# Optimization experiments

Hardware: AMD Instinct MI355X
Metric: run time of the kernel (lower is better)

## Reference

```python
import jax, jax.numpy as jnp
import numpy as np

DIM = 512
NUM_ITEM = 2048
K = 10


def setup_inputs() -> dict:
    key = jax.random.key(0)
    k1, k2, k3 = jax.random.split(key, 3)
    input1 = jax.random.normal(k1, (16, DIM, 32, 32), dtype=jnp.float32)
    input2 = jax.random.normal(k2, (16, DIM, 32, 32), dtype=jnp.float32)
    stdv = 1.0 / np.sqrt(DIM)
    mempool = jax.random.uniform(k3, (NUM_ITEM, DIM), minval=-stdv, maxval=stdv, dtype=jnp.float32)
    return {"input1": input1, "input2": input2, "mempool": mempool}


def _memorize(x, mempool):
    # x: [B, C, H, W] with C == DIM
    B, C, H, W = x.shape
    q = jnp.transpose(x, (0, 2, 3, 1)).reshape(-1, C)      # [N, C]
    att = jax.nn.softmax(q @ mempool.T, axis=1)            # [N, num_item]
    val, idx = jax.lax.top_k(att, K)                       # [N, K]
    val = jax.nn.softmax(val, axis=1)                      # renormalize top-k
    # scatter(val into zeros) @ mempool == gather rows of mempool and combine
    out = jnp.einsum('nk,nkd->nd', val, mempool[idx])      # [N, C]
    return jnp.transpose(out.reshape(B, H, W, C), (0, 3, 1, 2))


def reference(input1, input2, mempool):
    return (_memorize(input1, mempool), _memorize(input2, mempool))
```

## Files before the change

### kernel.cpp

```cpp
#include <hip/hip_runtime.h>
#include <math.h>

typedef __attribute__((ext_vector_type(4))) float f4;
typedef __attribute__((ext_vector_type(8))) _Float16 f16x8;
typedef __attribute__((ext_vector_type(8))) short bf16x8;
typedef __attribute__((ext_vector_type(4))) unsigned short u16x4;
typedef unsigned int u32;
typedef unsigned short u16;

#define DIMC  512
#define NITEM 2048
#define TK    10
#define WSP   (NITEM * DIMC)
#define XWSP  (32 * DIMC * 1024)
#define QWS_OFF (3 * WSP)

#define TPB    512
#define PXB    64
#define RIT    256
#define NRND   8
#define NSLICE 16

#define MP_PL  16384
#define Q_B    49152
#define Q_PL   4096
#define SSTR   66
#define LDS_BYTES 67584
#define MV_F 0
#define MI_F 5120
#define MM_F 10240
#define MS_F 10752
#define WB_F 11264
#define IB_F 11904

#define QB_SZ  12288

#define KSWZ(i) (((i) ^ ((i) >> 2)) & 3)

union h16 { _Float16 h; u16 u; };

__device__ __forceinline__ u32 bf16_rne(float f) {
    u32 u = __float_as_uint(f);
    return (u + 0x7fffu + ((u >> 16) & 1u)) >> 16;
}

__device__ __forceinline__ void split3(float f, u16& ph, u16& pb, u16& pr) {
    h16 a; a.h = (_Float16)f;
    float f0 = (float)a.h;
    ph = a.u;
    pb = (u16)bf16_rne(f);
    pr = (u16)bf16_rne(f - f0);
}

__global__ __launch_bounds__(256)
void preconv_kernel(const float* __restrict__ mp, u16* __restrict__ ws)
{
    int idx = (blockIdx.x * 256 + threadIdx.x) * 4;
    int i  = idx >> 9;
    int k0 = idx & 511;
    f4 v = *(const f4*)(mp + (size_t)i * 512 + k0);
    int s  = k0 >> 5, kl = k0 & 31;
    int lh = (kl >> 2) & 3, pair = kl >> 4;
    u16x4 pH, pB, pR;
#pragma unroll
    for (int e = 0; e < 4; ++e) {
        u16 h, b, r; split3(v[e], h, b, r);
        pH[e] = h; pB[e] = b; pR[e] = r;
    }
    size_t base = (size_t)(i >> 4) * 8192 + (size_t)s * 512
                + (size_t)(lh * 16 + (i & 15)) * 8 + pair * 4;
    *(u16x4*)(ws + 0 * WSP + base) = pH;
    *(u16x4*)(ws + 1 * WSP + base) = pB;
    *(u16x4*)(ws + 2 * WSP + base) = pR;
}

__global__ __launch_bounds__(256)
void preconv_x_kernel(const float* __restrict__ x0, const float* __restrict__ x1,
                      u16* __restrict__ ws)
{
    int T   = blockIdx.x * 256 + threadIdx.x;
    int px  = T & 1023;
    int c4  = (T >> 10) & 127;
    int img = T >> 17;
    const float* x = (img < 16) ? x0 : x1;
    const float* src = x + ((size_t)(img & 15) * 512 + (size_t)c4 * 4) * 1024 + px;
    int s = c4 >> 3, pair = (c4 >> 2) & 1, lh = c4 & 3;
    u16x4 pH, pB, pR;
#pragma unroll
    for (int j = 0; j < 4; ++j) {
        u16 h, b, r; split3(src[(size_t)j * 1024], h, b, r);
        pH[j] = h; pB[j] = b; pR[j] = r;
    }
    size_t base = (size_t)QWS_OFF
                + (size_t)(img * 64 + (px >> 4)) * 8192 + (size_t)s * 512
                + (size_t)((lh * 16 + (px & 15)) << 3) + pair * 4;
    *(u16x4*)(ws + base + 0 * (size_t)XWSP) = pH;
    *(u16x4*)(ws + base + 1 * (size_t)XWSP) = pB;
    *(u16x4*)(ws + base + 2 * (size_t)XWSP) = pR;
}

__global__ __launch_bounds__(TPB, 4)
void memorize_v11(const float* __restrict__ mp, const u16* __restrict__ ws,
                  float* __restrict__ out)
{
    extern __shared__ char ldsb[];
    float* ldsf = (float*)ldsb;

    const int t    = threadIdx.x;
    const int lane = t & 63;
    const int w    = t >> 6;
    const int blk  = blockIdx.x;
    const int img  = blk >> 4;
    const int n0   = (blk & 15) * PXB;

    float* ob = out + (img < 16 ? (size_t)0 : (size_t)16 * DIMC * 1024)
                    + (size_t)(img & 15) * (DIMC * 1024);

    const int l15 = lane & 15;
    const int lh  = lane >> 4;
    const int ksw = lh ^ KSWZ(l15);

    const int qp = t & 63;
    const int g  = t >> 6;

    float tv[TK]; int tix[TK];
#pragma unroll
    for (int q = 0; q < TK; ++q) { tv[q] = -INFINITY; tix[q] = 0x7fffffff; }
    float rm = -INFINITY, rs = 0.0f;

    const int permL = ((((lane & 3) ^ KSWZ(lane >> 2)) << 4) + (lane >> 2)) << 3;

    const int Gx = img * 64 + (blk & 15) * 4 + w;
    const u16* bsrc0 = ws + (size_t)QWS_OFF + ((size_t)Gx << 13) + permL;

    const char* qb = ldsb + Q_B + (l15 << 6) + (ksw << 4);
    const char* ab = ldsb + (size_t)((w << 5) + l15) * 64 + (ksw << 4);

#pragma unroll 1
    for (int r = 0; r < NRND; ++r) {
        f4 acc[2][4];
#pragma unroll
        for (int mt = 0; mt < 2; ++mt)
#pragma unroll
            for (int nt = 0; nt < 4; ++nt) acc[mt][nt] = (f4){0.f, 0.f, 0.f, 0.f};

#pragma unroll 1
        for (int s = 0; s < NSLICE; ++s) {
            __syncthreads();

#pragma unroll
            for (int p = 0; p < 3; ++p) {
#pragma unroll
                for (int gg = 0; gg < 2; ++gg) {
                    const u16* src = ws + (size_t)p * WSP
                                   + ((size_t)(r * 16 + w * 2 + gg) << 13)
                                   + (s << 9) + permL;
                    char* dst = ldsb + p * MP_PL + ((w << 5) + (gg << 4)) * 64;
                    __builtin_amdgcn_global_load_lds(
                        (const __attribute__((address_space(1))) u32*)src,
                        (__attribute__((address_space(3))) u32*)dst, 16, 0, 0);
                }
            }
            if (w < 4) {
#pragma unroll
                for (int p = 0; p < 3; ++p) {
                    const u16* src = bsrc0 + (size_t)p * XWSP + (s << 9);
                    char* dst = ldsb + Q_B + p * Q_PL + (w << 10);
                    __builtin_amdgcn_global_load_lds(
                        (const __attribute__((address_space(1))) u32*)src,
                        (__attribute__((address_space(3))) u32*)dst, 16, 0, 0);
                }
            }
            __syncthreads();

            f16x8  bqH[4];
            bf16x8 bqB[4], bqR[4];
#pragma unroll
            for (int nt = 0; nt < 4; ++nt) {
                bqH[nt] = *(const f16x8*) (qb + 0 * Q_PL + nt * 1024);
                bqB[nt] = *(const bf16x8*)(qb + 1 * Q_PL + nt * 1024);
                bqR[nt] = *(const bf16x8*)(qb + 2 * Q_PL + nt * 1024);
            }
#pragma unroll
            for (int mt = 0; mt < 2; ++mt) {
                f16x8  aH = *(const f16x8*) (ab + 0 * MP_PL + mt * 1024);
                bf16x8 aB = *(const bf16x8*)(ab + 1 * MP_PL + mt * 1024);
                bf16x8 aR = *(const bf16x8*)(ab + 2 * MP_PL + mt * 1024);
#pragma unroll
                for (int nt = 0; nt < 4; ++nt) {
                    f4 c = acc[mt][nt];
                    c = __builtin_amdgcn_mfma_f32_16x16x32_f16 (aH, bqH[nt], c, 0, 0, 0);
                    c = __builtin_amdgcn_mfma_f32_16x16x32_bf16(aB, bqR[nt], c, 0, 0, 0);
                    c = __builtin_amdgcn_mfma_f32_16x16x32_bf16(aR, bqB[nt], c, 0, 0, 0);
                    acc[mt][nt] = c;
                }
            }
        }

        __syncthreads();
#pragma unroll
        for (int mt = 0; mt < 2; ++mt) {
#pragma unroll
            for (int nt = 0; nt < 4; ++nt) {
                int row = (w << 5) + (mt << 4) + (lh << 2);
                int col = (nt << 4) + l15;
                float* sp = ldsf + row * SSTR + col;
                sp[0 * SSTR] = acc[mt][nt][0];
                sp[1 * SSTR] = acc[mt][nt][1];
                sp[2 * SSTR] = acc[mt][nt][2];
                sp[3 * SSTR] = acc[mt][nt][3];
            }
        }
        __syncthreads();

        float mloc = rm;
#pragma unroll 4
        for (int jj = 0; jj < 32; ++jj) {
            int   il = (g << 5) + jj;
            float v  = ldsf[il * SSTR + qp];
            mloc = fmaxf(mloc, v);
            if (v > tv[TK - 1]) {
                int   id = r * RIT + il;
                float cv = v; int ci = id;
#pragma unroll
                for (int q = 0; q < TK; ++q) {
                    bool  gt = cv > tv[q];
                    float nv = gt ? tv[q]  : cv;
                    int   ni = gt ? tix[q] : ci;
                    tv[q]  = gt ? cv : tv[q];
                    tix[q] = gt ? ci : tix[q];
                    cv = nv; ci = ni;
                }
            }
        }
        rs *= __expf(rm - mloc);
        rm = mloc;
#pragma unroll 4
        for (int jj = 0; jj < 32; ++jj) {
            int   il = (g << 5) + jj;
            float v  = ldsf[il * SSTR + qp];
            rs += __expf(v - rm);
        }
    }

    __syncthreads();
    {
#pragma unroll
        for (int q = 0; q < TK; ++q) {
            ldsf[MV_F + (qp * 8 + g) * TK + q] = tv[q];
            ldsf[MI_F + (qp * 8 + g) * TK + q] = __int_as_float(tix[q]);
        }
        ldsf[MM_F + qp * 8 + g] = rm;
        ldsf[MS_F + qp * 8 + g] = rs;
    }
    __syncthreads();

    if (t < 64) {
        const int p = t;
        float gm[8], gs[8];
#pragma unroll
        for (int G = 0; G < 8; ++G) {
            gm[G] = ldsf[MM_F + p * 8 + G];
            gs[G] = ldsf[MS_F + p * 8 + G];
        }
        float mstar = gm[0];
#pragma unroll
        for (int G = 1; G < 8; ++G) mstar = fmaxf(mstar, gm[G]);
        float Z = 0.0f;
#pragma unroll
        for (int G = 0; G < 8; ++G) Z += gs[G] * __expf(gm[G] - mstar);

        int h0=0,h1=0,h2=0,h3=0,h4=0,h5=0,h6=0,h7=0;
        float ov[TK]; int oi[TK];
#pragma unroll
        for (int o = 0; o < TK; ++o) {
            float bv = -INFINITY; int bi = 0x7fffffff; int bg = 0;
#define SEL(G, HG)                                                               \
            {                                                                    \
                float v  = ldsf[MV_F + (p * 8 + G) * TK + (HG)];                 \
                int   id = __float_as_int(ldsf[MI_F + (p * 8 + G) * TK + (HG)]); \
                if (v > bv || (v == bv && id < bi)) { bv = v; bi = id; bg = G; } \
            }
            SEL(0, h0) SEL(1, h1) SEL(2, h2) SEL(3, h3)
            SEL(4, h4) SEL(5, h5) SEL(6, h6) SEL(7, h7)
#undef SEL
            ov[o] = bv; oi[o] = bi;
            h0 += (bg == 0); h1 += (bg == 1); h2 += (bg == 2); h3 += (bg == 3);
            h4 += (bg == 4); h5 += (bg == 5); h6 += (bg == 6); h7 += (bg == 7);
        }
        float pv[TK];
#pragma unroll
        for (int o = 0; o < TK; ++o) pv[o] = __expf(ov[o] - mstar) / Z;
        float pmax = pv[0];
        float wgt[TK]; float W = 0.0f;
#pragma unroll
        for (int o = 0; o < TK; ++o) { wgt[o] = __expf(pv[o] - pmax); W += wgt[o]; }
#pragma unroll
        for (int o = 0; o < TK; ++o) {
            ldsf[WB_F + p * TK + o] = wgt[o] / W;
            ldsf[IB_F + p * TK + o] = __int_as_float(oi[o]);
        }
    }
    __syncthreads();

    {
        const int ep = t & 63, cg = t >> 6;
        float wr[TK]; const float* rows[TK];
#pragma unroll
        for (int o = 0; o < TK; ++o) {
            wr[o]   = ldsf[WB_F + ep * TK + o];
            rows[o] = mp + (size_t)__float_as_int(ldsf[IB_F + ep * TK + o]) * DIMC;
        }
        float* obase = ob + n0 + ep;
#pragma unroll 4
        for (int cc = 0; cc < 16; ++cc) {
            int c = cg * 64 + cc * 4;
            f4 a = {0.0f, 0.0f, 0.0f, 0.0f};
#pragma unroll
            for (int o = 0; o < TK; ++o) {
                f4 rv = *(const f4*)(rows[o] + c);
#pragma unroll
                for (int z = 0; z < 4; ++z) a[z] = fmaf(wr[o], rv[z], a[z]);
            }
#pragma unroll
            for (int z = 0; z < 4; ++z) obase[(size_t)(c + z) * 1024] = a[z];
        }
    }
}

__global__ __launch_bounds__(TPB, 4)
void memorize_fb(const float* __restrict__ x0, const float* __restrict__ x1,
                 const float* __restrict__ mp, const u16* __restrict__ ws,
                 float* __restrict__ out)
{
    extern __shared__ char ldsb[];
    float* ldsf = (float*)ldsb;

    const int t    = threadIdx.x;
    const int lane = t & 63;
    const int w    = t >> 6;
    const int blk  = blockIdx.x;
    const int img  = blk >> 4;
    const int n0   = (blk & 15) * PXB;
    const int b    = img & 15;

    const float* x  = (img < 16) ? x0 : x1;
    const float* xb = x + (size_t)b * (DIMC * 1024);
    float* ob = out + (img < 16 ? (size_t)0 : (size_t)16 * DIMC * 1024)
                    + (size_t)b * (DIMC * 1024);

    const int l15 = lane & 15;
    const int lh  = lane >> 4;
    const int ksw = lh ^ KSWZ(l15);
    const int ig  = w >> 1;
    const int pg  = w & 1;
    const int qp = t & 63;
    const int g  = t >> 6;

    float tv[TK]; int tix[TK];
#pragma unroll
    for (int q = 0; q < TK; ++q) { tv[q] = -INFINITY; tix[q] = 0x7fffffff; }
    float rm = -INFINITY, rs = 0.0f;

    const int scl  = t & 31;
    const int spx  = (t >> 5) << 2;
    const int spos = (((scl >> 2) & 3) << 3) + ((scl >> 4) << 2) + (scl & 3);
    const int sslot = spos >> 3;
    const int soff  = (spos & 7) << 1;

    const u16* aw = ws + (size_t)lane * 8 + (size_t)(ig * 4) * 8192;
    const int qfb = (pg << 11) + (l15 << 6) + (ksw << 4);

#define STAGE_Q(S, BUF)                                                        \
    {                                                                          \
        const float* src = xb + (size_t)(((S) << 5) + scl) * 1024 + n0 + spx;  \
        f4 v = *(const f4*)src;                                                \
        _Pragma("unroll")                                                      \
        for (int e = 0; e < 4; ++e) {                                          \
            int px = spx + e;                                                  \
            u16 h, bb, rr; split3(v[e], h, bb, rr);                            \
            int ro = (BUF) * QB_SZ + (px << 6)                                 \
                   + (((sslot ^ KSWZ(px)) << 4) | soff);                       \
            *(u16*)(ldsb + ro)            = h;                                 \
            *(u16*)(ldsb + ro + Q_PL)     = bb;                                \
            *(u16*)(ldsb + ro + 2 * Q_PL) = rr;                                \
        }                                                                      \
    }

#define ALOADF(IT, S)                                                          \
    {                                                                          \
        const u16* ap = ar + ((size_t)(IT) << 13) + ((S) << 9);                \
        aH[IT] = *(const f16x8*) (ap + 0 * WSP);                               \
        aB[IT] = *(const bf16x8*)(ap + 1 * WSP);                               \
        aR[IT] = *(const bf16x8*)(ap + 2 * WSP);                               \
    }

#pragma unroll 1
    for (int r = 0; r < NRND; ++r) {
        const u16* ar = aw + ((size_t)r << 17);
        f4 acc[4][2];
#pragma unroll
        for (int it = 0; it < 4; ++it)
#pragma unroll
            for (int pt = 0; pt < 2; ++pt) acc[it][pt] = (f4){0.f, 0.f, 0.f, 0.f};

        __syncthreads();
        STAGE_Q(0, 0)
        __syncthreads();

#pragma unroll 1
        for (int s = 0; s < NSLICE; ++s) {
            const int cur = s & 1;
            f16x8 aH[4]; bf16x8 aB[4], aR[4];
            ALOADF(0, s)
            ALOADF(1, s)
            if (s + 1 < NSLICE) STAGE_Q(s + 1, cur ^ 1)

            const char* qc = ldsb + cur * QB_SZ + qfb;
            f16x8 qH[2]; bf16x8 qB[2], qR[2];
#pragma unroll
            for (int pt = 0; pt < 2; ++pt) {
                qH[pt] = *(const f16x8*) (qc + 0 * Q_PL + pt * 1024);
                qB[pt] = *(const bf16x8*)(qc + 1 * Q_PL + pt * 1024);
                qR[pt] = *(const bf16x8*)(qc + 2 * Q_PL + pt * 1024);
            }
#pragma unroll
            for (int it = 0; it < 4; ++it) {
                if (it < 2) ALOADF(it + 2, s)
#pragma unroll
                for (int pt = 0; pt < 2; ++pt) {
                    f4 c = acc[it][pt];
                    c = __builtin_amdgcn_mfma_f32_16x16x32_f16 (aH[it], qH[pt], c, 0, 0, 0);
                    c = __builtin_amdgcn_mfma_f32_16x16x32_bf16(aB[it], qR[pt], c, 0, 0, 0);
                    c = __builtin_amdgcn_mfma_f32_16x16x32_bf16(aR[it], qB[pt], c, 0, 0, 0);
                    acc[it][pt] = c;
                }
            }
            __syncthreads();
        }

#pragma unroll
        for (int it = 0; it < 4; ++it) {
#pragma unroll
            for (int pt = 0; pt < 2; ++pt) {
                int row = (ig << 6) + (it << 4) + (lh << 2);
                int col = (pg << 5) + (pt << 4) + l15;
                float* sp = ldsf + row * SSTR + col;
                sp[0 * SSTR] = acc[it][pt][0];
                sp[1 * SSTR] = acc[it][pt][1];
                sp[2 * SSTR] = acc[it][pt][2];
                sp[3 * SSTR] = acc[it][pt][3];
            }
        }
        __syncthreads();

        float mloc = rm;
#pragma unroll 4
        for (int jj = 0; jj < 32; ++jj) {
            int   il = (g << 5) + jj;
            float v  = ldsf[il * SSTR + qp];
            mloc = fmaxf(mloc, v);
            if (v > tv[TK - 1]) {
                int   id = r * RIT + il;
                float cv = v; int ci = id;
#pragma unroll
                for (int q = 0; q < TK; ++q) {
                    bool  gt = cv > tv[q];
                    float nv = gt ? tv[q]  : cv;
                    int   ni = gt ? tix[q] : ci;
                    tv[q]  = gt ? cv : tv[q];
                    tix[q] = gt ? ci : tix[q];
                    cv = nv; ci = ni;
                }
            }
        }
        rs *= __expf(rm - mloc);
        rm = mloc;
#pragma unroll 4
        for (int jj = 0; jj < 32; ++jj) {
            int   il = (g << 5) + jj;
            float v  = ldsf[il * SSTR + qp];
            rs += __expf(v - rm);
        }
    }
#undef STAGE_Q
#undef ALOADF

    __syncthreads();
    {
#pragma unroll
        for (int q = 0; q < TK; ++q) {
            ldsf[MV_F + (qp * 8 + g) * TK + q] = tv[q];
            ldsf[MI_F + (qp * 8 + g) * TK + q] = __int_as_float(tix[q]);
        }
        ldsf[MM_F + qp * 8 + g] = rm;
        ldsf[MS_F + qp * 8 + g] = rs;
    }
    __syncthreads();

    if (t < 64) {
        const int p = t;
        float gm[8], gs[8];
#pragma unroll
        for (int G = 0; G < 8; ++G) {
            gm[G] = ldsf[MM_F + p * 8 + G];
            gs[G] = ldsf[MS_F + p * 8 + G];
        }
        float mstar = gm[0];
#pragma unroll
        for (int G = 1; G < 8; ++G) mstar = fmaxf(mstar, gm[G]);
        float Z = 0.0f;
#pragma unroll
        for (int G = 0; G < 8; ++G) Z += gs[G] * __expf(gm[G] - mstar);

        int h0=0,h1=0,h2=0,h3=0,h4=0,h5=0,h6=0,h7=0;
        float ov[TK]; int oi[TK];
#pragma unroll
        for (int o = 0; o < TK; ++o) {
            float bv = -INFINITY; int bi = 0x7fffffff; int bg = 0;
#define SEL(G, HG)                                                               \
            {                                                                    \
                float v  = ldsf[MV_F + (p * 8 + G) * TK + (HG)];                 \
                int   id = __float_as_int(ldsf[MI_F + (p * 8 + G) * TK + (HG)]); \
                if (v > bv || (v == bv && id < bi)) { bv = v; bi = id; bg = G; } \
            }
            SEL(0, h0) SEL(1, h1) SEL(2, h2) SEL(3, h3)
            SEL(4, h4) SEL(5, h5) SEL(6, h6) SEL(7, h7)
#undef SEL
            ov[o] = bv; oi[o] = bi;
            h0 += (bg == 0); h1 += (bg == 1); h2 += (bg == 2); h3 += (bg == 3);
            h4 += (bg == 4); h5 += (bg == 5); h6 += (bg == 6); h7 += (bg == 7);
        }
        float pv[TK];
#pragma unroll
        for (int o = 0; o < TK; ++o) pv[o] = __expf(ov[o] - mstar) / Z;
        float pmax = pv[0];
        float wgt[TK]; float W = 0.0f;
#pragma unroll
        for (int o = 0; o < TK; ++o) { wgt[o] = __expf(pv[o] - pmax); W += wgt[o]; }
#pragma unroll
        for (int o = 0; o < TK; ++o) {
            ldsf[WB_F + p * TK + o] = wgt[o] / W;
            ldsf[IB_F + p * TK + o] = __int_as_float(oi[o]);
        }
    }
    __syncthreads();

    {
        const int ep = t & 63, cg = t >> 6;
        float wr[TK]; const float* rows[TK];
#pragma unroll
        for (int o = 0; o < TK; ++o) {
            wr[o]   = ldsf[WB_F + ep * TK + o];
            rows[o] = mp + (size_t)__float_as_int(ldsf[IB_F + ep * TK + o]) * DIMC;
        }
        float* obase = ob + n0 + ep;
#pragma unroll 4
        for (int cc = 0; cc < 16; ++cc) {
            int c = cg * 64 + cc * 4;
            f4 a = {0.0f, 0.0f, 0.0f, 0.0f};
#pragma unroll
            for (int o = 0; o < TK; ++o) {
                f4 rv = *(const f4*)(rows[o] + c);
#pragma unroll
                for (int z = 0; z < 4; ++z) a[z] = fmaf(wr[o], rv[z], a[z]);
            }
#pragma unroll
            for (int z = 0; z < 4; ++z) obase[(size_t)(c + z) * 1024] = a[z];
        }
    }
}

extern "C" void kernel_launch(void* const* d_in, const int* in_sizes, int n_in,
                              void* d_out, int out_size, void* d_ws, size_t ws_size,
                              hipStream_t stream) {
    const float* x0  = (const float*)d_in[0];
    const float* x1  = (const float*)d_in[1];
    const float* mpl = (const float*)d_in[2];
    float* out = (float*)d_out;
    u16* ws = (u16*)d_ws;

    const size_t ws_need = ((size_t)QWS_OFF + 3ull * (size_t)XWSP) * 2ull;

    preconv_kernel<<<dim3(1024), dim3(256), 0, stream>>>(mpl, ws);
    if (ws_size >= ws_need) {
        preconv_x_kernel<<<dim3(16384), dim3(256), 0, stream>>>(x0, x1, ws);
        memorize_v11<<<dim3(512), dim3(TPB), LDS_BYTES, stream>>>(mpl, ws, out);
    } else {
        memorize_fb<<<dim3(512), dim3(TPB), LDS_BYTES, stream>>>(x0, x1, mpl, ws, out);
    }
}
```

Measured before the change: 612.9 us.

## Prefetch next mempool slice and load query fragments directly from global

```diff
diff --git a/kernel.cpp b/kernel.cpp
--- a/kernel.cpp
+++ b/kernel.cpp
@@ -22,8 +22,6 @@
 #define NSLICE 16
 
 #define MP_PL  16384
-#define Q_B    49152
-#define Q_PL   4096
 #define SSTR   66
 #define LDS_BYTES 67584
 #define MV_F 0
@@ -34,6 +32,7 @@
 #define IB_F 11904
 
 #define QB_SZ  12288
+#define Q_PL   4096
 
 #define KSWZ(i) (((i) ^ ((i) >> 2)) & 3)
 
@@ -100,7 +99,7 @@
 }
 
 __global__ __launch_bounds__(TPB, 4)
-void memorize_v11(const float* __restrict__ mp, const u16* __restrict__ ws,
+void memorize_v12(const float* __restrict__ mp, const u16* __restrict__ ws,
                   float* __restrict__ out)
 {
     extern __shared__ char ldsb[];
@@ -130,11 +129,27 @@
 
     const int permL = ((((lane & 3) ^ KSWZ(lane >> 2)) << 4) + (lane >> 2)) << 3;
 
-    const int Gx = img * 64 + (blk & 15) * 4 + w;
-    const u16* bsrc0 = ws + (size_t)QWS_OFF + ((size_t)Gx << 13) + permL;
-
-    const char* qb = ldsb + Q_B + (l15 << 6) + (ksw << 4);
+    const int G0 = img * 64 + (blk & 15) * 4;
+    const u16* bw = ws + (size_t)QWS_OFF + ((size_t)G0 << 13) + (size_t)lane * 8;
+
     const char* ab = ldsb + (size_t)((w << 5) + l15) * 64 + (ksw << 4);
+
+#define STAGE_A(R, S)                                                          \
+    {                                                                          \
+        _Pragma("unroll")                                                      \
+        for (int p = 0; p < 3; ++p) {                                          \
+            _Pragma("unroll")                                                  \
+            for (int gg = 0; gg < 2; ++gg) {                                   \
+                const u16* src = ws + (size_t)p * WSP                          \
+                               + ((size_t)((R) * 16 + w * 2 + gg) << 13)       \
+                               + ((S) << 9) + permL;                           \
+                char* dst = ldsb + p * MP_PL + ((w << 5) + (gg << 4)) * 64;    \
+                __builtin_amdgcn_global_load_lds(                              \
+                    (const __attribute__((address_space(1))) u32*)src,         \
+                    (__attribute__((address_space(3))) u32*)dst, 16, 0, 0);    \
+            }                                                                  \
+        }                                                                      \
+    }
 
 #pragma unroll 1
     for (int r = 0; r < NRND; ++r) {
@@ -144,55 +159,49 @@
 #pragma unroll
             for (int nt = 0; nt < 4; ++nt) acc[mt][nt] = (f4){0.f, 0.f, 0.f, 0.f};
 
+        __syncthreads();
+        STAGE_A(r, 0)
+
 #pragma unroll 1
         for (int s = 0; s < NSLICE; ++s) {
-            __syncthreads();
-
-#pragma unroll
-            for (int p = 0; p < 3; ++p) {
-#pragma unroll
-                for (int gg = 0; gg < 2; ++gg) {
-                    const u16* src = ws + (size_t)p * WSP
-                                   + ((size_t)(r * 16 + w * 2 + gg) << 13)
-                                   + (s << 9) + permL;
-                    char* dst = ldsb + p * MP_PL + ((w << 5) + (gg << 4)) * 64;
-                    __builtin_amdgcn_global_load_lds(
-                        (const __attribute__((address_space(1))) u32*)src,
-                        (__attribute__((address_space(3))) u32*)dst, 16, 0, 0);
+            asm volatile("s_waitcnt vmcnt(0)" ::: "memory");
+            __builtin_amdgcn_sched_barrier(0);
+
+            f16x8 aH[2]; bf16x8 aB[2], aR[2];
+#pragma unroll
+            for (int mt = 0; mt < 2; ++mt) {
+                aH[mt] = *(const f16x8*) (ab + 0 * MP_PL + mt * 1024);
+                aB[mt] = *(const bf16x8*)(ab + 1 * MP_PL + mt * 1024);
+                aR[mt] = *(const bf16x8*)(ab + 2 * MP_PL + mt * 1024);
+            }
+            asm volatile("s_waitcnt lgkmcnt(0)" ::: "memory");
+            __builtin_amdgcn_sched_barrier(0);
+
+            if (s + 1 < NSLICE) STAGE_A(r, s + 1)
+            __builtin_amdgcn_sched_barrier(0);
+
+            const u16* bs = bw + ((size_t)s << 9);
+#pragma unroll
+            for (int nh = 0; nh < 2; ++nh) {
+                f16x8 bqH[2]; bf16x8 bqB[2], bqR[2];
+#pragma unroll
+                for (int j = 0; j < 2; ++j) {
+                    const u16* bp = bs + ((size_t)(nh * 2 + j) << 13);
+                    bqH[j] = *(const f16x8*) (bp);
+                    bqB[j] = *(const bf16x8*)(bp + (size_t)XWSP);
+                    bqR[j] = *(const bf16x8*)(bp + 2 * (size_t)XWSP);
                 }
-            }
-            if (w < 4) {
-#pragma unroll
-                for (int p = 0; p < 3; ++p) {
-                    const u16* src = bsrc0 + (size_t)p * XWSP + (s << 9);
-                    char* dst = ldsb + Q_B + p * Q_PL + (w << 10);
-                    __builtin_amdgcn_global_load_lds(
-                        (const __attribute__((address_space(1))) u32*)src,
-                        (__attribute__((address_space(3))) u32*)dst, 16, 0, 0);
-                }
-            }
-            __syncthreads();
-
-            f16x8  bqH[4];
-            bf16x8 bqB[4], bqR[4];
-#pragma unroll
-            for (int nt = 0; nt < 4; ++nt) {
-                bqH[nt] = *(const f16x8*) (qb + 0 * Q_PL + nt * 1024);
-                bqB[nt] = *(const bf16x8*)(qb + 1 * Q_PL + nt * 1024);
-                bqR[nt] = *(const bf16x8*)(qb + 2 * Q_PL + nt * 1024);
-            }
-#pragma unroll
-            for (int mt = 0; mt < 2; ++mt) {
-                f16x8  aH = *(const f16x8*) (ab + 0 * MP_PL + mt * 1024);
-                bf16x8 aB = *(const bf16x8*)(ab + 1 * MP_PL + mt * 1024);
-                bf16x8 aR = *(const bf16x8*)(ab + 2 * MP_PL + mt * 1024);
-#pragma unroll
-                for (int nt = 0; nt < 4; ++nt) {
-                    f4 c = acc[mt][nt];
-                    c = __builtin_amdgcn_mfma_f32_16x16x32_f16 (aH, bqH[nt], c, 0, 0, 0);
-                    c = __builtin_amdgcn_mfma_f32_16x16x32_bf16(aB, bqR[nt], c, 0, 0, 0);
-                    c = __builtin_amdgcn_mfma_f32_16x16x32_bf16(aR, bqB[nt], c, 0, 0, 0);
-                    acc[mt][nt] = c;
+#pragma unroll
+                for (int j = 0; j < 2; ++j) {
+                    int nt = nh * 2 + j;
+#pragma unroll
+                    for (int mt = 0; mt < 2; ++mt) {
+                        f4 c = acc[mt][nt];
+                        c = __builtin_amdgcn_mfma_f32_16x16x32_f16 (aH[mt], bqH[j], c, 0, 0, 0);
+                        c = __builtin_amdgcn_mfma_f32_16x16x32_bf16(aB[mt], bqR[j], c, 0, 0, 0);
+                        c = __builtin_amdgcn_mfma_f32_16x16x32_bf16(aR[mt], bqB[j], c, 0, 0, 0);
+                        acc[mt][nt] = c;
+                    }
                 }
             }
         }
@@ -242,6 +251,7 @@
             rs += __expf(v - rm);
         }
     }
+#undef STAGE_A
 
     __syncthreads();
     {
@@ -585,7 +595,7 @@
     preconv_kernel<<<dim3(1024), dim3(256), 0, stream>>>(mpl, ws);
     if (ws_size >= ws_need) {
         preconv_x_kernel<<<dim3(16384), dim3(256), 0, stream>>>(x0, x1, ws);
-        memorize_v11<<<dim3(512), dim3(TPB), LDS_BYTES, stream>>>(mpl, ws, out);
+        memorize_v12<<<dim3(512), dim3(TPB), LDS_BYTES, stream>>>(mpl, ws, out);
     } else {
         memorize_fb<<<dim3(512), dim3(TPB), LDS_BYTES, stream>>>(x0, x1, mpl, ws, out);
     }
```

After: 805.6 us. 1.31x slower.
